# Kernel tuning notes

Hardware: AMD Instinct MI355X
Metric: run time of the kernel (lower is better)

The kernel has to match this reference:

```python
import jax, jax.numpy as jnp
import numpy as np

N = 262144
IN_DIM = 64
HID = 256
EMB = 128
OUT = 64
B = 16
MAX_AISLES = 64
NUM_SEG = B * MAX_AISLES  # static upper bound on number of (batch, aisle) segments


def setup_inputs() -> dict:
    key = jax.random.key(0)
    ks = jax.random.split(key, 16)
    def lin(k, fan_in, fan_out):
        bound = 1.0 / np.sqrt(fan_in)
        kw, kb = jax.random.split(k)
        W = jax.random.uniform(kw, (fan_in, fan_out), jnp.float32, -bound, bound)
        b = jax.random.uniform(kb, (fan_out,), jnp.float32, -bound, bound)
        return W, b
    W1, b1 = lin(ks[0], IN_DIM, HID)
    W2, b2 = lin(ks[1], HID, HID)
    W3, b3 = lin(ks[2], HID, EMB)
    A1, c1 = lin(ks[3], 2 * EMB, HID)
    A2, c2 = lin(ks[4], HID, HID)
    A3, c3 = lin(ks[5], HID, OUT)
    x = jax.random.normal(ks[6], (N, IN_DIM), jnp.float32)
    aisle_nrs = jax.random.randint(ks[7], (N,), 0, MAX_AISLES, jnp.int32)
    batch = jnp.sort(jax.random.randint(ks[8], (N,), 0, B, jnp.int32))
    return {"x": x, "aisle_nrs": aisle_nrs, "batch": batch,
            "W1": W1, "b1": b1, "W2": W2, "b2": b2, "W3": W3, "b3": b3,
            "A1": A1, "c1": c1, "A2": A2, "c2": c2, "A3": A3, "c3": c3}


def reference(x, aisle_nrs, batch, W1, b1, W2, b2, W3, b3, A1, c1, A2, c2, A3, c3):
    lrelu = lambda v: jax.nn.leaky_relu(v, 0.01)  # torch LeakyReLU default slope
    h = lrelu(x @ W1 + b1)
    h = lrelu(h @ W2 + b2)
    h = h @ W3 + b3  # [N, EMB]
    # dynamic group id: aisle + batch * (max_aisle + 1)
    aisle_ids = aisle_nrs + batch * (jnp.max(aisle_nrs) + 1)
    # scatter-mean over segments (NUM_SEG is a static upper bound)
    sums = jax.ops.segment_sum(h, aisle_ids, num_segments=NUM_SEG)
    counts = jax.ops.segment_sum(jnp.ones((h.shape[0],), h.dtype), aisle_ids,
                                 num_segments=NUM_SEG)
    means = sums / jnp.maximum(counts, 1.0)[:, None]
    # gather back and concat
    z = jnp.concatenate([h, means[aisle_ids]], axis=1)  # [N, 2*EMB]
    z = lrelu(z @ A1 + c1)
    z = lrelu(z @ A2 + c2)
    z = z @ A3 + c3
    return z
```

## Files before the change

### kernel.cpp

```cpp
#include <hip/hip_runtime.h>
#include <hip/hip_bf16.h>

#define N_ROWS 262144
#define IN_DIM 64
#define HID 256
#define EMB 128
#define OUT_DIM 64
#define NSEG 1024
#define ROWS_B 128
#define MT 8
#define NWAVE 8
#define LDS_S 264
#define CHUNK 1024
#define NSLOTS (2 * (N_ROWS / CHUNK))

typedef _Float16 h16;
typedef _Float16 h16x8 __attribute__((ext_vector_type(8)));
typedef _Float16 h16x4 __attribute__((ext_vector_type(4)));
typedef float f32x4 __attribute__((ext_vector_type(4)));


__global__ void k_max(const int* __restrict__ aisle, int* __restrict__ maxA) {
    int v = 0;
    for (int i = blockIdx.x * blockDim.x + threadIdx.x; i < N_ROWS; i += gridDim.x * blockDim.x)
        v = max(v, aisle[i]);
#pragma unroll
    for (int off = 32; off > 0; off >>= 1) v = max(v, __shfl_down(v, off));
    __shared__ int red[4];
    if ((threadIdx.x & 63) == 0) red[threadIdx.x >> 6] = v;
    __syncthreads();
    if (threadIdx.x == 0) {
        int m = red[0];
        for (int i = 1; i < 4; ++i) m = max(m, red[i]);
        atomicMax(maxA, m);
    }
}

__device__ __forceinline__ void frag_nk(int o, int K, int& n, int& k) {
    int tile = o / (16 * K);
    int r = o - tile * 16 * K;
    n = tile * 16 + ((r >> 3) & 15);
    k = (r >> 9) * 32 + (((r >> 7) & 3) << 3) + (r & 7);
}

__global__ void k_prep_weights(const float* __restrict__ W1, const float* __restrict__ W2,
                               const float* __restrict__ W3, const float* __restrict__ A1f,
                               const float* __restrict__ A2f, const float* __restrict__ A3f,
                               h16* __restrict__ W1t, h16* __restrict__ W2t, h16* __restrict__ W3t,
                               h16* __restrict__ A1t, h16* __restrict__ A2t, h16* __restrict__ A3t) {
    int idx = blockIdx.x * 256 + threadIdx.x;
    int n, k;
    if (idx < 16384)       { int o = idx;          frag_nk(o, 64, n, k);  W1t[o] = (h16)W1[k * 256 + n]; }
    else if (idx < 81920)  { int o = idx - 16384;  frag_nk(o, 256, n, k); W2t[o] = (h16)W2[k * 256 + n]; }
    else if (idx < 114688) { int o = idx - 81920;  frag_nk(o, 256, n, k); W3t[o] = (h16)W3[k * 128 + n]; }
    else if (idx < 180224) { int o = idx - 114688; frag_nk(o, 256, n, k); A1t[o] = (h16)A1f[k * 256 + n]; }
    else if (idx < 245760) { int o = idx - 180224; frag_nk(o, 256, n, k); A2t[o] = (h16)A2f[k * 256 + n]; }
    else                   { int o = idx - 245760; frag_nk(o, 256, n, k); A3t[o] = (h16)A3f[k * 64  + n]; }
}

template <int K, int NOUT, bool ACT>
__device__ __forceinline__ void mlp_layer_ip(const h16* __restrict__ Wt,
                                             const float* __restrict__ bias,
                                             h16* __restrict__ S,
                                             int lane, int wave) {
    constexpr int NW = NOUT / NWAVE;
    constexpr int NT = NW / 16;
    constexpr int KT = K / 32;
    const int l15 = lane & 15, l4 = lane >> 4;
    f32x4 acc[MT][NT];
#pragma unroll
    for (int mt = 0; mt < MT; ++mt)
#pragma unroll
        for (int nt = 0; nt < NT; ++nt)
#pragma unroll
            for (int j = 0; j < 4; ++j) acc[mt][nt][j] = 0.f;

    const h16* wb[NT];
#pragma unroll
    for (int nt = 0; nt < NT; ++nt)
        wb[nt] = Wt + (size_t)(wave * NT + nt) * 16 * K + lane * 8;

    h16x8 b0[NT], b1[NT], b2[NT];
#pragma unroll
    for (int nt = 0; nt < NT; ++nt) b0[nt] = *(const h16x8*)wb[nt];
    if (KT > 1) {
#pragma unroll
        for (int nt = 0; nt < NT; ++nt) b1[nt] = *(const h16x8*)(wb[nt] + 512);
    }
    if (KT > 2) {
#pragma unroll
        for (int nt = 0; nt < NT; ++nt) b2[nt] = *(const h16x8*)(wb[nt] + 1024);
    }

#pragma unroll
    for (int kt = 0; kt < KT; ++kt) {
        h16x8 bc[NT];
#pragma unroll
        for (int nt = 0; nt < NT; ++nt) bc[nt] = b0[nt];
#pragma unroll
        for (int nt = 0; nt < NT; ++nt) b0[nt] = b1[nt];
#pragma unroll
        for (int nt = 0; nt < NT; ++nt) b1[nt] = b2[nt];
        if (kt + 3 < KT) {
#pragma unroll
            for (int nt = 0; nt < NT; ++nt) b2[nt] = *(const h16x8*)(wb[nt] + (kt + 3) * 512);
        }
        __builtin_amdgcn_s_setprio(1);
#pragma unroll
        for (int mt = 0; mt < MT; ++mt) {
            h16x8 a = *(const h16x8*)&S[(mt * 16 + l15) * LDS_S + kt * 32 + l4 * 8];
#pragma unroll
            for (int nt = 0; nt < NT; ++nt)
                acc[mt][nt] = __builtin_amdgcn_mfma_f32_16x16x32_f16(bc[nt], a, acc[mt][nt], 0, 0, 0);
        }
        __builtin_amdgcn_s_setprio(0);
    }

    __syncthreads();

#pragma unroll
    for (int nt = 0; nt < NT; ++nt) {
        const int cb = wave * NW + nt * 16 + l4 * 4;
        const f32x4 bias4 = *(const f32x4*)&bias[cb];
#pragma unroll
        for (int mt = 0; mt < MT; ++mt) {
            f32x4 v = acc[mt][nt] + bias4;
            if (ACT) {
#pragma unroll
                for (int j = 0; j < 4; ++j) v[j] = fmaxf(v[j], 0.01f * v[j]);
            }
            h16x4 hv;
#pragma unroll
            for (int j = 0; j < 4; ++j) hv[j] = (h16)v[j];
            *(h16x4*)&S[(mt * 16 + l15) * LDS_S + cb] = hv;
        }
    }
    __syncthreads();
}

__device__ __forceinline__ void mlp_layer_out_h16(const h16* __restrict__ Wt,
                                                  const float* __restrict__ bias,
                                                  const h16* __restrict__ S,
                                                  h16* __restrict__ gout, int row0,
                                                  int lane, int wave) {
    const int l15 = lane & 15, l4 = lane >> 4;
    f32x4 acc[MT];
#pragma unroll
    for (int mt = 0; mt < MT; ++mt)
#pragma unroll
        for (int j = 0; j < 4; ++j) acc[mt][j] = 0.f;

    const h16* wb = Wt + (size_t)wave * 16 * 256 + lane * 8;
    h16x8 b0 = *(const h16x8*)wb;
    h16x8 b1 = *(const h16x8*)(wb + 512);
    h16x8 b2 = *(const h16x8*)(wb + 1024);
#pragma unroll
    for (int kt = 0; kt < 8; ++kt) {
        h16x8 bc = b0;
        b0 = b1;
        b1 = b2;
        if (kt + 3 < 8) b2 = *(const h16x8*)(wb + (kt + 3) * 512);
        __builtin_amdgcn_s_setprio(1);
#pragma unroll
        for (int mt = 0; mt < MT; ++mt) {
            h16x8 a = *(const h16x8*)&S[(mt * 16 + l15) * LDS_S + kt * 32 + l4 * 8];
            acc[mt] = __builtin_amdgcn_mfma_f32_16x16x32_f16(bc, a, acc[mt], 0, 0, 0);
        }
        __builtin_amdgcn_s_setprio(0);
    }

    const int cb = wave * 16 + l4 * 4;
    const f32x4 bias4 = *(const f32x4*)&bias[cb];
#pragma unroll
    for (int mt = 0; mt < MT; ++mt) {
        f32x4 v = acc[mt] + bias4;
        h16x4 hv;
#pragma unroll
        for (int j = 0; j < 4; ++j) hv[j] = (h16)v[j];
        *(h16x4*)&gout[(size_t)(row0 + mt * 16 + l15) * 128 + cb] = hv;
    }
}

__global__ __launch_bounds__(512, 4) void k1(const float* __restrict__ x,
                                             const h16* __restrict__ W1t, const float* __restrict__ b1,
                                             const h16* __restrict__ W2t, const float* __restrict__ b2,
                                             const h16* __restrict__ W3t, const float* __restrict__ b3,
                                             h16* __restrict__ hbuf) {
    __shared__ __align__(16) h16 S[ROWS_B * LDS_S];
    const int tid = threadIdx.x, lane = tid & 63, wave = tid >> 6;
    const int row0 = blockIdx.x * ROWS_B;

    {
        const int r = tid >> 2, c16 = (tid & 3) * 16;
        const float* src = &x[(size_t)(row0 + r) * 64 + c16];
        f32x4 v0 = *(const f32x4*)&src[0];
        f32x4 v1 = *(const f32x4*)&src[4];
        f32x4 v2 = *(const f32x4*)&src[8];
        f32x4 v3 = *(const f32x4*)&src[12];
        h16x8 h0, h1;
#pragma unroll
        for (int j = 0; j < 4; ++j) { h0[j] = (h16)v0[j]; h0[4 + j] = (h16)v1[j];
                                      h1[j] = (h16)v2[j]; h1[4 + j] = (h16)v3[j]; }
        *(h16x8*)&S[r * LDS_S + c16]     = h0;
        *(h16x8*)&S[r * LDS_S + c16 + 8] = h1;
    }
    __syncthreads();

    mlp_layer_ip<64, 256, true>(W1t, b1, S, lane, wave);
    mlp_layer_ip<256, 256, true>(W2t, b2, S, lane, wave);
    mlp_layer_out_h16(W3t, b3, S, hbuf, row0, lane, wave);
}

__global__ __launch_bounds__(512) void k_scatter(const h16* __restrict__ hbuf,
                                                 const int* __restrict__ aisle,
                                                 const int* __restrict__ batch,
                                                 float* __restrict__ partials,
                                                 float* __restrict__ pcount,
                                                 int* __restrict__ bvmap) {
    __shared__ int la[CHUNK], lb[CHUNK], rankv[CHUNK], rowlist[CHUNK];
    __shared__ int hist[128], scan[128];
    const int tid = threadIdx.x;
    const int row0 = blockIdx.x * CHUNK;

    if (tid < 128) hist[tid] = 0;
    for (int i = tid; i < CHUNK; i += 512) { la[i] = aisle[row0 + i]; lb[i] = batch[row0 + i]; }
    __syncthreads();

    const int bLo = lb[0], bHi = lb[CHUNK - 1];

    for (int i = tid; i < CHUNK; i += 512) {
        int slot = min(lb[i] - bLo, 1);
        rankv[i] = atomicAdd(&hist[slot * 64 + la[i]], 1);
    }
    __syncthreads();
    if (tid < 128) scan[tid] = hist[tid];
    __syncthreads();
#pragma unroll
    for (int st = 1; st < 128; st <<= 1) {
        int v = 0;
        if (tid < 128 && tid >= st) v = scan[tid - st];
        __syncthreads();
        if (tid < 128) scan[tid] += v;
        __syncthreads();
    }
    for (int i = tid; i < CHUNK; i += 512) {
        int bin = min(lb[i] - bLo, 1) * 64 + la[i];
        rowlist[scan[bin] - hist[bin] + rankv[i]] = i;
    }
    __syncthreads();

    const int a_own = tid >> 3, cg = tid & 7;
    for (int slot = 0; slot < 2; ++slot) {
        const int sid = blockIdx.x * 2 + slot;
        const int bv = bLo + slot;
        if (bv > bHi) { if (tid == 0) bvmap[sid] = -1; continue; }

        const int bin = slot * 64 + a_own;
        const int s1 = scan[bin];
        const int s0 = s1 - hist[bin];

        float acc[16];
#pragma unroll
        for (int j = 0; j < 16; ++j) acc[j] = 0.f;

        for (int idx = s0; idx < s1; ++idx) {
            const int r = rowlist[idx];
            const h16x8* src = (const h16x8*)&hbuf[(size_t)(row0 + r) * 128 + cg * 16];
            h16x8 v0 = src[0], v1 = src[1];
#pragma unroll
            for (int j = 0; j < 8; ++j) {
                acc[j]     += (float)v0[j];
                acc[8 + j] += (float)v1[j];
            }
        }
        float* dst = &partials[(size_t)sid * 8192 + a_own * 128 + cg * 16];
#pragma unroll
        for (int g2 = 0; g2 < 4; ++g2) *(f32x4*)&dst[g2 * 4] = *(const f32x4*)&acc[g2 * 4];
        if (cg == 0) pcount[sid * 64 + a_own] = (float)(s1 - s0);
        if (tid == 0) bvmap[sid] = bv;
    }
}

__global__ __launch_bounds__(128) void k_means(const float* __restrict__ partials,
                                               const float* __restrict__ pcount,
                                               const int* __restrict__ bvmap,
                                               h16* __restrict__ means,
                                               const int* __restrict__ maxA) {
    __shared__ int sbv[NSLOTS];
    __shared__ int lohi[2];
    const int b = blockIdx.x >> 6, a = blockIdx.x & 63;
    const int tid = threadIdx.x;
    const int mult = *maxA + 1;
    for (int i = tid; i < NSLOTS; i += 128) sbv[i] = bvmap[i];
    if (tid == 0) { lohi[0] = NSLOTS; lohi[1] = 0; }
    __syncthreads();
    int llo = NSLOTS, lhi = 0;
#pragma unroll
    for (int q = 0; q < 4; ++q) {
        const int i = tid * 4 + q;
        if (sbv[i] == b) { if (i < llo) llo = i; lhi = i + 1; }
    }
    if (llo < NSLOTS) atomicMin(&lohi[0], llo);
    if (lhi > 0)      atomicMax(&lohi[1], lhi);
    __syncthreads();
    if (a >= mult) return;

    float sum = 0.f, cnt = 0.f;
    for (int s = lohi[0]; s < lohi[1]; ++s) {
        if (sbv[s] == b) {
            sum += partials[(size_t)s * 8192 + a * 128 + tid];
            cnt += pcount[s * 64 + a];
        }
    }
    means[(size_t)(b * mult + a) * 128 + tid] = (h16)(sum / fmaxf(cnt, 1.0f));
}

__global__ __launch_bounds__(512, 4) void k3(const h16* __restrict__ hbuf,
                                             const int* __restrict__ aisle,
                                             const int* __restrict__ batch,
                                             const h16* __restrict__ means,
                                             const h16* __restrict__ A1t, const float* __restrict__ c1,
                                             const h16* __restrict__ A2t, const float* __restrict__ c2,
                                             const h16* __restrict__ A3t, const float* __restrict__ c3,
                                             float* __restrict__ out, const int* __restrict__ maxA) {
    __shared__ __align__(16) h16 S[ROWS_B * LDS_S];
    const int tid = threadIdx.x, lane = tid & 63, wave = tid >> 6;
    const int row0 = blockIdx.x * ROWS_B;
    const int mult = *maxA + 1;

    {
        const int r = tid >> 2, p = tid & 3;
        const int g = row0 + r;
        const h16x8* hs = (const h16x8*)&hbuf[(size_t)g * 128 + p * 32];
        h16x8* hd = (h16x8*)&S[r * LDS_S + p * 32];
        hd[0] = hs[0]; hd[1] = hs[1]; hd[2] = hs[2]; hd[3] = hs[3];
        const int id = aisle[g] + batch[g] * mult;
        const h16x8* ms = (const h16x8*)&means[(size_t)id * 128 + p * 32];
        h16x8* md = (h16x8*)&S[r * LDS_S + 128 + p * 32];
        md[0] = ms[0]; md[1] = ms[1]; md[2] = ms[2]; md[3] = ms[3];
    }
    __syncthreads();

    mlp_layer_ip<256, 256, true>(A1t, c1, S, lane, wave);
    mlp_layer_ip<256, 256, true>(A2t, c2, S, lane, wave);

    {
        const int l15 = lane & 15, l4 = lane >> 4;
        const int w4 = wave & 3, kw = wave >> 2;
        f32x4 acc4[MT];
#pragma unroll
        for (int mt = 0; mt < MT; ++mt)
#pragma unroll
            for (int j = 0; j < 4; ++j) acc4[mt][j] = 0.f;

        const h16* wb = A3t + (size_t)w4 * 16 * 256 + (size_t)kw * 4 * 512 + lane * 8;
        h16x8 b0 = *(const h16x8*)wb;
        h16x8 b1 = *(const h16x8*)(wb + 512);
        h16x8 b2 = *(const h16x8*)(wb + 1024);
#pragma unroll
        for (int kt = 0; kt < 4; ++kt) {
            h16x8 bc = b0;
            b0 = b1;
            b1 = b2;
            if (kt + 3 < 4) b2 = *(const h16x8*)(wb + (kt + 3) * 512);
            __builtin_amdgcn_s_setprio(1);
#pragma unroll
            for (int mt = 0; mt < MT; ++mt) {
                h16x8 a = *(const h16x8*)&S[(mt * 16 + l15) * LDS_S + kw * 128 + kt * 32 + l4 * 8];
                acc4[mt] = __builtin_amdgcn_mfma_f32_16x16x32_f16(bc, a, acc4[mt], 0, 0, 0);
            }
            __builtin_amdgcn_s_setprio(0);
        }
        __syncthreads();
        float* fS = (float*)S;
        if (kw == 1) {
#pragma unroll
            for (int mt = 0; mt < MT; ++mt) {
                const int row = mt * 16 + l15;
                *(f32x4*)&fS[row * 68 + w4 * 16 + l4 * 4] = acc4[mt];
            }
        }
        __syncthreads();
        if (kw == 0) {
            const f32x4 bias4 = *(const f32x4*)&c3[w4 * 16 + l4 * 4];
#pragma unroll
            for (int mt = 0; mt < MT; ++mt) {
                const int row = mt * 16 + l15;
                f32x4 p = *(const f32x4*)&fS[row * 68 + w4 * 16 + l4 * 4];
                f32x4 v = acc4[mt] + p + bias4;
                *(f32x4*)&out[(size_t)(row0 + row) * 64 + w4 * 16 + l4 * 4] = v;
            }
        }
    }
}

extern "C" void kernel_launch(void* const* d_in, const int* in_sizes, int n_in,
                              void* d_out, int out_size, void* d_ws, size_t ws_size,
                              hipStream_t stream) {
    const float* x     = (const float*)d_in[0];
    const int*   aisle = (const int*)d_in[1];
    const int*   batch = (const int*)d_in[2];
    const float* W1 = (const float*)d_in[3];  const float* b1 = (const float*)d_in[4];
    const float* W2 = (const float*)d_in[5];  const float* b2 = (const float*)d_in[6];
    const float* W3 = (const float*)d_in[7];  const float* b3 = (const float*)d_in[8];
    const float* A1 = (const float*)d_in[9];  const float* c1 = (const float*)d_in[10];
    const float* A2 = (const float*)d_in[11]; const float* c2 = (const float*)d_in[12];
    const float* A3 = (const float*)d_in[13]; const float* c3 = (const float*)d_in[14];
    float* out = (float*)d_out;

    char* w = (char*)d_ws;
    size_t off = 0;
    h16*   hbuf     = (h16*)(w + off);   off += (size_t)N_ROWS * 128 * sizeof(h16);
    float* partials = (float*)(w + off); off += (size_t)NSLOTS * 8192 * sizeof(float);
    float* pcount   = (float*)(w + off); off += NSLOTS * 64 * sizeof(float);
    int*   bvmap    = (int*)(w + off);   off += NSLOTS * sizeof(int);
    h16*   means    = (h16*)(w + off);   off += NSEG * 128 * sizeof(h16);
    h16*   W1t      = (h16*)(w + off);   off += 16384 * sizeof(h16);
    h16*   W2t      = (h16*)(w + off);   off += 65536 * sizeof(h16);
    h16*   W3t      = (h16*)(w + off);   off += 32768 * sizeof(h16);
    h16*   A1t      = (h16*)(w + off);   off += 65536 * sizeof(h16);
    h16*   A2t      = (h16*)(w + off);   off += 65536 * sizeof(h16);
    h16*   A3t      = (h16*)(w + off);   off += 16384 * sizeof(h16);
    int*   maxA     = (int*)(w + off);   off += 256;

    hipMemsetAsync(maxA, 0, sizeof(int), stream);

    k_max<<<256, 256, 0, stream>>>(aisle, maxA);
    k_prep_weights<<<1024, 256, 0, stream>>>(W1, W2, W3, A1, A2, A3, W1t, W2t, W3t, A1t, A2t, A3t);
    k1<<<N_ROWS / ROWS_B, 512, 0, stream>>>(x, W1t, b1, W2t, b2, W3t, b3, hbuf);
    k_scatter<<<N_ROWS / CHUNK, 512, 0, stream>>>(hbuf, aisle, batch, partials, pcount, bvmap);
    k_means<<<16 * 64, 128, 0, stream>>>(partials, pcount, bvmap, means, maxA);
    k3<<<N_ROWS / ROWS_B, 512, 0, stream>>>(hbuf, aisle, batch, means, A1t, c1, A2t, c2, A3t, c3,
                                            out, maxA);
}
```

Baseline: 317.7 us.

## Double row tile to 256 with 2x4 wave grid for weight reuse

```diff
diff --git a/kernel.cpp b/kernel.cpp
--- a/kernel.cpp
+++ b/kernel.cpp
@@ -7,7 +7,7 @@
 #define EMB 128
 #define OUT_DIM 64
 #define NSEG 1024
-#define ROWS_B 128
+#define ROWS_B 256
 #define MT 8
 #define NWAVE 8
 #define LDS_S 264
@@ -58,15 +58,16 @@
     else                   { int o = idx - 245760; frag_nk(o, 256, n, k); A3t[o] = (h16)A3f[k * 64  + n]; }
 }
 
-template <int K, int NOUT, bool ACT>
+template <int K, bool ACT>
 __device__ __forceinline__ void mlp_layer_ip(const h16* __restrict__ Wt,
                                              const float* __restrict__ bias,
                                              h16* __restrict__ S,
                                              int lane, int wave) {
-    constexpr int NW = NOUT / NWAVE;
-    constexpr int NT = NW / 16;
+    constexpr int NT = 4;
     constexpr int KT = K / 32;
     const int l15 = lane & 15, l4 = lane >> 4;
+    const int rg = wave >> 2, cg = wave & 3;
+    const int rbase = rg * 128;
     f32x4 acc[MT][NT];
 #pragma unroll
     for (int mt = 0; mt < MT; ++mt)
@@ -78,19 +79,15 @@
     const h16* wb[NT];
 #pragma unroll
     for (int nt = 0; nt < NT; ++nt)
-        wb[nt] = Wt + (size_t)(wave * NT + nt) * 16 * K + lane * 8;
-
-    h16x8 b0[NT], b1[NT], b2[NT];
+        wb[nt] = Wt + (size_t)(cg * NT + nt) * 16 * K + lane * 8;
+
+    h16x8 b0[NT], b1[NT];
 #pragma unroll
     for (int nt = 0; nt < NT; ++nt) b0[nt] = *(const h16x8*)wb[nt];
     if (KT > 1) {
 #pragma unroll
         for (int nt = 0; nt < NT; ++nt) b1[nt] = *(const h16x8*)(wb[nt] + 512);
     }
-    if (KT > 2) {
-#pragma unroll
-        for (int nt = 0; nt < NT; ++nt) b2[nt] = *(const h16x8*)(wb[nt] + 1024);
-    }
 
 #pragma unroll
     for (int kt = 0; kt < KT; ++kt) {
@@ -99,16 +96,14 @@
         for (int nt = 0; nt < NT; ++nt) bc[nt] = b0[nt];
 #pragma unroll
         for (int nt = 0; nt < NT; ++nt) b0[nt] = b1[nt];
-#pragma unroll
-        for (int nt = 0; nt < NT; ++nt) b1[nt] = b2[nt];
-        if (kt + 3 < KT) {
-#pragma unroll
-            for (int nt = 0; nt < NT; ++nt) b2[nt] = *(const h16x8*)(wb[nt] + (kt + 3) * 512);
+        if (kt + 2 < KT) {
+#pragma unroll
+            for (int nt = 0; nt < NT; ++nt) b1[nt] = *(const h16x8*)(wb[nt] + (kt + 2) * 512);
         }
         __builtin_amdgcn_s_setprio(1);
 #pragma unroll
         for (int mt = 0; mt < MT; ++mt) {
-            h16x8 a = *(const h16x8*)&S[(mt * 16 + l15) * LDS_S + kt * 32 + l4 * 8];
+            h16x8 a = *(const h16x8*)&S[(rbase + mt * 16 + l15) * LDS_S + kt * 32 + l4 * 8];
 #pragma unroll
             for (int nt = 0; nt < NT; ++nt)
                 acc[mt][nt] = __builtin_amdgcn_mfma_f32_16x16x32_f16(bc[nt], a, acc[mt][nt], 0, 0, 0);
@@ -120,7 +115,7 @@
 
 #pragma unroll
     for (int nt = 0; nt < NT; ++nt) {
-        const int cb = wave * NW + nt * 16 + l4 * 4;
+        const int cb = cg * 64 + nt * 16 + l4 * 4;
         const f32x4 bias4 = *(const f32x4*)&bias[cb];
 #pragma unroll
         for (int mt = 0; mt < MT; ++mt) {
@@ -132,7 +127,7 @@
             h16x4 hv;
 #pragma unroll
             for (int j = 0; j < 4; ++j) hv[j] = (h16)v[j];
-            *(h16x4*)&S[(mt * 16 + l15) * LDS_S + cb] = hv;
+            *(h16x4*)&S[(rbase + mt * 16 + l15) * LDS_S + cb] = hv;
         }
     }
     __syncthreads();
@@ -144,44 +139,63 @@
                                                   h16* __restrict__ gout, int row0,
                                                   int lane, int wave) {
     const int l15 = lane & 15, l4 = lane >> 4;
-    f32x4 acc[MT];
+    const int rg = wave >> 2, cg = wave & 3;
+    const int rbase = rg * 128;
+    f32x4 acc[MT][2];
 #pragma unroll
     for (int mt = 0; mt < MT; ++mt)
 #pragma unroll
-        for (int j = 0; j < 4; ++j) acc[mt][j] = 0.f;
-
-    const h16* wb = Wt + (size_t)wave * 16 * 256 + lane * 8;
-    h16x8 b0 = *(const h16x8*)wb;
-    h16x8 b1 = *(const h16x8*)(wb + 512);
-    h16x8 b2 = *(const h16x8*)(wb + 1024);
+        for (int nt = 0; nt < 2; ++nt)
+#pragma unroll
+            for (int j = 0; j < 4; ++j) acc[mt][nt][j] = 0.f;
+
+    const h16* wb[2];
+#pragma unroll
+    for (int nt = 0; nt < 2; ++nt)
+        wb[nt] = Wt + (size_t)(cg * 2 + nt) * 16 * 256 + lane * 8;
+
+    h16x8 b0[2], b1[2];
+#pragma unroll
+    for (int nt = 0; nt < 2; ++nt) { b0[nt] = *(const h16x8*)wb[nt];
+                                     b1[nt] = *(const h16x8*)(wb[nt] + 512); }
 #pragma unroll
     for (int kt = 0; kt < 8; ++kt) {
-        h16x8 bc = b0;
-        b0 = b1;
-        b1 = b2;
-        if (kt + 3 < 8) b2 = *(const h16x8*)(wb + (kt + 3) * 512);
+        h16x8 bc[2];
+#pragma unroll
+        for (int nt = 0; nt < 2; ++nt) bc[nt] = b0[nt];
+#pragma unroll
+        for (int nt = 0; nt < 2; ++nt) b0[nt] = b1[nt];
+        if (kt + 2 < 8) {
+#pragma unroll
+            for (int nt = 0; nt < 2; ++nt) b1[nt] = *(const h16x8*)(wb[nt] + (kt + 2) * 512);
+        }
         __builtin_amdgcn_s_setprio(1);
 #pragma unroll
         for (int mt = 0; mt < MT; ++mt) {
-            h16x8 a = *(const h16x8*)&S[(mt * 16 + l15) * LDS_S + kt * 32 + l4 * 8];
-            acc[mt] = __builtin_amdgcn_mfma_f32_16x16x32_f16(bc, a, acc[mt], 0, 0, 0);
+            h16x8 a = *(const h16x8*)&S[(rbase + mt * 16 + l15) * LDS_S + kt * 32 + l4 * 8];
+#pragma unroll
+            for (int nt = 0; nt < 2; ++nt)
+                acc[mt][nt] = __builtin_amdgcn_mfma_f32_16x16x32_f16(bc[nt], a, acc[mt][nt], 0, 0, 0);
         }
         __builtin_amdgcn_s_setprio(0);
     }
 
-    const int cb = wave * 16 + l4 * 4;
-    const f32x4 bias4 = *(const f32x4*)&bias[cb];
-#pragma unroll
-    for (int mt = 0; mt < MT; ++mt) {
-        f32x4 v = acc[mt] + bias4;
-        h16x4 hv;
-#pragma unroll
-        for (int j = 0; j < 4; ++j) hv[j] = (h16)v[j];
-        *(h16x4*)&gout[(size_t)(row0 + mt * 16 + l15) * 128 + cb] = hv;
-    }
-}
-
-__global__ __launch_bounds__(512, 4) void k1(const float* __restrict__ x,
+#pragma unroll
+    for (int nt = 0; nt < 2; ++nt) {
+        const int cb = cg * 32 + nt * 16 + l4 * 4;
+        const f32x4 bias4 = *(const f32x4*)&bias[cb];
+#pragma unroll
+        for (int mt = 0; mt < MT; ++mt) {
+            f32x4 v = acc[mt][nt] + bias4;
+            h16x4 hv;
+#pragma unroll
+            for (int j = 0; j < 4; ++j) hv[j] = (h16)v[j];
+            *(h16x4*)&gout[(size_t)(row0 + rbase + mt * 16 + l15) * 128 + cb] = hv;
+        }
+    }
+}
+
+__global__ __launch_bounds__(512, 2) void k1(const float* __restrict__ x,
                                              const h16* __restrict__ W1t, const float* __restrict__ b1,
                                              const h16* __restrict__ W2t, const float* __restrict__ b2,
                                              const h16* __restrict__ W3t, const float* __restrict__ b3,
@@ -190,8 +204,8 @@
     const int tid = threadIdx.x, lane = tid & 63, wave = tid >> 6;
     const int row0 = blockIdx.x * ROWS_B;
 
-    {
-        const int r = tid >> 2, c16 = (tid & 3) * 16;
+    for (int i = tid; i < 1024; i += 512) {
+        const int r = i >> 2, c16 = (i & 3) * 16;
         const float* src = &x[(size_t)(row0 + r) * 64 + c16];
         f32x4 v0 = *(const f32x4*)&src[0];
         f32x4 v1 = *(const f32x4*)&src[4];
@@ -206,8 +220,8 @@
     }
     __syncthreads();
 
-    mlp_layer_ip<64, 256, true>(W1t, b1, S, lane, wave);
-    mlp_layer_ip<256, 256, true>(W2t, b2, S, lane, wave);
+    mlp_layer_ip<64, true>(W1t, b1, S, lane, wave);
+    mlp_layer_ip<256, true>(W2t, b2, S, lane, wave);
     mlp_layer_out_h16(W3t, b3, S, hbuf, row0, lane, wave);
 }
 
@@ -315,7 +329,7 @@
     means[(size_t)(b * mult + a) * 128 + tid] = (h16)(sum / fmaxf(cnt, 1.0f));
 }
 
-__global__ __launch_bounds__(512, 4) void k3(const h16* __restrict__ hbuf,
+__global__ __launch_bounds__(512, 2) void k3(const h16* __restrict__ hbuf,
                                              const int* __restrict__ aisle,
                                              const int* __restrict__ batch,
                                              const h16* __restrict__ means,
@@ -328,8 +342,8 @@
     const int row0 = blockIdx.x * ROWS_B;
     const int mult = *maxA + 1;
 
-    {
-        const int r = tid >> 2, p = tid & 3;
+    for (int i = tid; i < 1024; i += 512) {
+        const int r = i >> 2, p = i & 3;
         const int g = row0 + r;
         const h16x8* hs = (const h16x8*)&hbuf[(size_t)g * 128 + p * 32];
         h16x8* hd = (h16x8*)&S[r * LDS_S + p * 32];
@@ -341,55 +355,40 @@
     }
     __syncthreads();
 
-    mlp_layer_ip<256, 256, true>(A1t, c1, S, lane, wave);
-    mlp_layer_ip<256, 256, true>(A2t, c2, S, lane, wave);
+    mlp_layer_ip<256, true>(A1t, c1, S, lane, wave);
+    mlp_layer_ip<256, true>(A2t, c2, S, lane, wave);
 
     {
         const int l15 = lane & 15, l4 = lane >> 4;
-        const int w4 = wave & 3, kw = wave >> 2;
+        const int rg = wave >> 2, cg = wave & 3;
+        const int rbase = rg * 128;
         f32x4 acc4[MT];
 #pragma unroll
         for (int mt = 0; mt < MT; ++mt)
 #pragma unroll
             for (int j = 0; j < 4; ++j) acc4[mt][j] = 0.f;
 
-        const h16* wb = A3t + (size_t)w4 * 16 * 256 + (size_t)kw * 4 * 512 + lane * 8;
+        const h16* wb = A3t + (size_t)cg * 16 * 256 + lane * 8;
         h16x8 b0 = *(const h16x8*)wb;
         h16x8 b1 = *(const h16x8*)(wb + 512);
-        h16x8 b2 = *(const h16x8*)(wb + 1024);
-#pragma unroll
-        for (int kt = 0; kt < 4; ++kt) {
+#pragma unroll
+        for (int kt = 0; kt < 8; ++kt) {
             h16x8 bc = b0;
             b0 = b1;
-            b1 = b2;
-            if (kt + 3 < 4) b2 = *(const h16x8*)(wb + (kt + 3) * 512);
+            if (kt + 2 < 8) b1 = *(const h16x8*)(wb + (kt + 2) * 512);
             __builtin_amdgcn_s_setprio(1);
 #pragma unroll
             for (int mt = 0; mt < MT; ++mt) {
-                h16x8 a = *(const h16x8*)&S[(mt * 16 + l15) * LDS_S + kw * 128 + kt * 32 + l4 * 8];
+                h16x8 a = *(const h16x8*)&S[(rbase + mt * 16 + l15) * LDS_S + kt * 32 + l4 * 8];
                 acc4[mt] = __builtin_amdgcn_mfma_f32_16x16x32_f16(bc, a, acc4[mt], 0, 0, 0);
             }
             __builtin_amdgcn_s_setprio(0);
         }
-        __syncthreads();
-        float* fS = (float*)S;
-        if (kw == 1) {
-#pragma unroll
-            for (int mt = 0; mt < MT; ++mt) {
-                const int row = mt * 16 + l15;
-                *(f32x4*)&fS[row * 68 + w4 * 16 + l4 * 4] = acc4[mt];
-            }
-        }
-        __syncthreads();
-        if (kw == 0) {
-            const f32x4 bias4 = *(const f32x4*)&c3[w4 * 16 + l4 * 4];
-#pragma unroll
-            for (int mt = 0; mt < MT; ++mt) {
-                const int row = mt * 16 + l15;
-                f32x4 p = *(const f32x4*)&fS[row * 68 + w4 * 16 + l4 * 4];
-                f32x4 v = acc4[mt] + p + bias4;
-                *(f32x4*)&out[(size_t)(row0 + row) * 64 + w4 * 16 + l4 * 4] = v;
-            }
+        const f32x4 bias4 = *(const f32x4*)&c3[cg * 16 + l4 * 4];
+#pragma unroll
+        for (int mt = 0; mt < MT; ++mt) {
+            f32x4 v = acc4[mt] + bias4;
+            *(f32x4*)&out[(size_t)(row0 + rbase + mt * 16 + l15) * 64 + cg * 16 + l4 * 4] = v;
         }
     }
 }
```

After: 343.9 us. 8.3% more time.
